# Performance work log

Hardware: AMD Instinct MI355X
Metric: run time of the kernel (lower is better)

Reference implementation:

```python
import jax, jax.numpy as jnp
import numpy as np

N_NODES = 100000
N_EDGES = 1600000
IN_CH, OUT_CH = 6, 32


def _glorot(key, shape):
    fan_in, fan_out = shape[0], shape[1]
    lim = float(np.sqrt(6.0 / (fan_in + fan_out)))
    return jax.random.uniform(key, shape, jnp.float32, -lim, lim)


def setup_inputs() -> dict:
    key = jax.random.key(0)
    ks = jax.random.split(key, 16)
    x = jax.random.normal(ks[0], (N_NODES, IN_CH), jnp.float32)
    edge_tp = jax.random.randint(ks[1], (2, N_EDGES), 0, N_NODES, jnp.int32)
    edge_int = jax.random.randint(ks[2], (2, N_EDGES), 0, N_NODES, jnp.int32)
    return {
        'x': x, 'edge_tp': edge_tp, 'edge_int': edge_int,
        # block 1 (6 -> 32): self lin, per-edge-type message lins, residual proj
        'W_self1': _glorot(ks[3], (IN_CH, OUT_CH)), 'b1': jnp.zeros((OUT_CH,), jnp.float32),
        'W_tp1': _glorot(ks[4], (IN_CH, OUT_CH)), 'W_int1': _glorot(ks[5], (IN_CH, OUT_CH)),
        'W_res1': _glorot(ks[6], (IN_CH, OUT_CH)),
        # block 2 (32 -> 32): identity residual
        'W_self2': _glorot(ks[7], (OUT_CH, OUT_CH)), 'b2': jnp.zeros((OUT_CH,), jnp.float32),
        'W_tp2': _glorot(ks[8], (OUT_CH, OUT_CH)), 'W_int2': _glorot(ks[9], (OUT_CH, OUT_CH)),
        # instance decoder MLP
        'Wd1': _glorot(ks[10], (OUT_CH, OUT_CH)), 'bd1': jnp.zeros((OUT_CH,), jnp.float32),
        'Wd2': _glorot(ks[11], (OUT_CH, 1)), 'bd2': jnp.zeros((1,), jnp.float32),
    }


def _hetero_block(x, edge_tp, edge_int, W_self, b, W_tp, W_int, W_res):
    """One ResidualGeneralHeteroConvBlock: per-edge-type message passing
    ('temp_previous' -> sum-agg, 'intersects' -> mean-agg) + self transform +
    residual, then ReLU. x: [N, Cin]."""
    N = x.shape[0]
    # temp_previous: add reducer
    src, dst = edge_tp[0], edge_tp[1]
    m_tp = jax.ops.segment_sum(x[src] @ W_tp, dst, num_segments=N)  # [N, Cout]
    # intersects: mean reducer
    s2, d2 = edge_int[0], edge_int[1]
    m_sum = jax.ops.segment_sum(x[s2] @ W_int, d2, num_segments=N)
    cnt = jax.ops.segment_sum(jnp.ones(d2.shape, x.dtype), d2, num_segments=N)
    m_int = m_sum / jnp.maximum(cnt, 1.0)[:, None]
    res = x @ W_res if W_res is not None else x
    return jax.nn.relu(x @ W_self + b + m_tp + m_int + res)


def reference(x, edge_tp, edge_int,
              W_self1, b1, W_tp1, W_int1, W_res1,
              W_self2, b2, W_tp2, W_int2,
              Wd1, bd1, Wd2, bd2):
    h = _hetero_block(x, edge_tp, edge_int, W_self1, b1, W_tp1, W_int1, W_res1)
    h = _hetero_block(h, edge_tp, edge_int, W_self2, b2, W_tp2, W_int2, None)
    # instance decoder: Linear -> ReLU -> Linear -> sigmoid
    h = jax.nn.relu(h @ Wd1 + bd1)
    return jax.nn.sigmoid(h @ Wd2 + bd2)  # [N, 1]
```

## Files before the change

kernel.cpp:

```cpp
#include <hip/hip_runtime.h>
#include <hip/hip_bf16.h>
#include <math.h>

#define NN   100000
#define ICH  6
#define OCH  32
#define NBK  782
#define PBLK 512
#define CAPB 4720
#define CAPL 4800
#define GN   16
#define CHMAX 6272

#define WPREP_N 4480

typedef float f32x2 __attribute__((ext_vector_type(2)));
typedef float f32x4 __attribute__((ext_vector_type(4)));

__device__ __forceinline__ void pk_fma(f32x2& a, f32x2 x, f32x2 y) {
    asm("v_pk_fma_f32 %0, %1, %2, %0" : "+v"(a) : "v"(x), "v"(y));
}
__device__ __forceinline__ f32x2 pk_add(f32x2 x, f32x2 y) {
    f32x2 d;
    asm("v_pk_add_f32 %0, %1, %2" : "=v"(d) : "v"(x), "v"(y));
    return d;
}

__device__ __forceinline__ float ldf(const void* p, long i, int f32) {
    return f32 ? ((const float*)p)[i]
               : __bfloat162float(((const __hip_bfloat16*)p)[i]);
}
__device__ __forceinline__ float lo16f(unsigned u) { return __uint_as_float(u << 16); }
__device__ __forceinline__ float hi16f(unsigned u) { return __uint_as_float(u & 0xFFFF0000u); }

__device__ __forceinline__ int binof(int n, int s) {
    return ((n >> 7) << 8) | (s << 7) | (n & 127);
}

__global__ __launch_bounds__(1024) void partAx_r25(
        const int* __restrict__ src_tp, const int* __restrict__ dst_tp,
        const int* __restrict__ src_int, const int* __restrict__ dst_int,
        int Etp, int E,
        const void* __restrict__ x, unsigned* __restrict__ xw,
        int* __restrict__ gcnt, unsigned* __restrict__ part,
        int* __restrict__ flagp,
        const void* Ws2, const void* b2v, const void* Wt2, const void* Wi2,
        const void* Wd1, const void* bd1v, const void* Wd2, const void* bd2v,
        float* __restrict__ wprep) {
    __shared__ unsigned rawv[CHMAX];
    __shared__ unsigned short rawb[CHMAX];
    __shared__ unsigned sorted[CHMAX];
    __shared__ int lh[NBK];
    __shared__ int cur[NBK];
    __shared__ int lofs[NBK + 1];
    __shared__ int wsum[16];
    __shared__ int weird;
    int t = threadIdx.x, blk = blockIdx.x;
    if (t == 0) weird = 0;
    for (int b = t; b < NBK; b += 1024) lh[b] = 0;
    __syncthreads();
    {
        const __hip_bfloat16* p = (const __hip_bfloat16*)x;
        int w = 0;
        for (int i = t; i < 4096; i += 1024) {
            float v = fabsf(__bfloat162float(p[i]));
            if (!(v <= 1000.0f) || (v > 0.0f && v < 1e-4f)) w++;
        }
        if (w) atomicAdd(&weird, w);
    }
    __syncthreads();
    int f32 = (weird > 500) ? 1 : 0;
    if (blk == 0 && t == 0) *flagp = f32;
    if (blk == 0) {
        for (int i = t; i < 96 * 32; i += 1024) {
            int k = i >> 5, c = i & 31;
            float w;
            if (k < 32)      w = ldf(Ws2, k * 32 + c, f32) + ((k == c) ? 1.0f : 0.0f);
            else if (k < 64) w = ldf(Wt2, (k - 32) * 32 + c, f32);
            else             w = ldf(Wi2, (k - 64) * 32 + c, f32);
            wprep[c * 100 + k] = w;
        }
        for (int i = t; i < 32 * 32; i += 1024) {
            int k = i >> 5, c = i & 31;
            wprep[3200 + c * 36 + k] = ldf(Wd1, k * 32 + c, f32);
        }
        if (t < 32) {
            wprep[4352 + t]      = ldf(b2v, t, f32);
            wprep[4352 + 32 + t] = ldf(bd1v, t, f32);
            wprep[4352 + 64 + t] = ldf(Wd2, t, f32);
        }
        if (t == 0) wprep[4352 + 96] = ldf(bd2v, 0, f32);
    }
    for (int w = blk * 1024 + t; w < NN * 4; w += PBLK * 1024) {
        int n = w >> 2, j = w & 3;
        int c0 = 2 * j, c1 = 2 * j + 1;
        __hip_bfloat16 v0 = (c0 < ICH) ? __float2bfloat16(ldf(x, (long)n * ICH + c0, f32))
                                       : __float2bfloat16(0.0f);
        __hip_bfloat16 v1 = (c1 < ICH) ? __float2bfloat16(ldf(x, (long)n * ICH + c1, f32))
                                       : __float2bfloat16(0.0f);
        xw[w] = (unsigned)__bfloat16_as_ushort(v0) |
                ((unsigned)__bfloat16_as_ushort(v1) << 16);
    }
    int CH = (E + PBLK - 1) / PBLK;
    int lo = blk * CH, hi = min(E, lo + CH);
    int n = hi - lo;
    for (int e = lo + t; e < hi; e += 1024) {
        int bin, src;
        if (e < Etp) { bin = binof(dst_tp[e], 0); src = src_tp[e]; }
        else         { bin = binof(dst_int[e - Etp], 1); src = src_int[e - Etp]; }
        int i = e - lo;
        rawv[i] = ((unsigned)(bin & 255) << 24) | (unsigned)src;
        rawb[i] = (unsigned short)(bin >> 8);
        atomicAdd(&lh[bin >> 8], 1);
    }
    __syncthreads();
    for (int b = t; b < NBK; b += 1024) {
        int cnt = lh[b];
        cur[b] = b * CAPB + (cnt ? atomicAdd(&gcnt[b], cnt) : 0);
    }
    {
        int v = (t < NBK) ? lh[t] : 0;
        int lane = t & 63, w = t >> 6;
        int s = v;
#pragma unroll
        for (int d = 1; d < 64; d <<= 1) {
            int u = __shfl_up(s, d, 64);
            if (lane >= d) s += u;
        }
        if (lane == 63) wsum[w] = s;
        __syncthreads();
        int prefix = 0;
#pragma unroll
        for (int j = 0; j < 16; ++j) prefix += (j < w) ? wsum[j] : 0;
        int excl = prefix + s - v;
        if (t < NBK) {
            lofs[t] = excl;
            cur[t] -= excl;
            lh[t]  = excl;
        }
        if (t == 0) lofs[NBK] = n;
        __syncthreads();
    }
    for (int i = t; i < n; i += 1024) {
        int b = rawb[i];
        int pos = atomicAdd(&lh[b], 1);
        sorted[pos] = rawv[i];
    }
    __syncthreads();
    {
        int grp = t >> 3, lane8 = t & 7;
        for (int b = grp; b < NBK; b += 128) {
            int st = lofs[b], en = lofs[b + 1];
            int dst = cur[b];
            for (int i = st + lane8; i < en; i += 8)
                part[dst + i] = sorted[i];
        }
    }
}

__global__ __launch_bounds__(256) void passBn1_r25(
        unsigned* __restrict__ partcsr, const int* __restrict__ gcnt,
        int* __restrict__ off, int* __restrict__ end,
        const unsigned* __restrict__ xw,
        const void* Ws1, const void* b1v, const void* Wt1, const void* Wi1, const void* Wr1,
        unsigned* __restrict__ h1u, float* __restrict__ invc_a,
        const int* __restrict__ flag) {
    __shared__ unsigned lp[CAPL];
    __shared__ unsigned sorted[CAPL];
    __shared__ int scnt[256], obin[256];
    __shared__ int wsum4[4];
    __shared__ float agg[256][7];
    __shared__ float sWs[ICH][32], sWt[ICH][32], sWi[ICH][32];
    __shared__ float sb1[32];
    int k = blockIdx.x, t = threadIdx.x;
    int f32 = *flag;
    if (k == 0 && t < 16) h1u[(size_t)NN * 16u + t] = 0u;
    if (t < ICH * OCH) {
        int kk = t >> 5, c = t & 31;
        sWs[kk][c] = ldf(Ws1, t, f32) + ldf(Wr1, t, f32);
        sWt[kk][c] = ldf(Wt1, t, f32);
        sWi[kk][c] = ldf(Wi1, t, f32);
    }
    if (t < 32) sb1[t] = ldf(b1v, t, f32);
    int s0 = k * CAPB;
    int cnt = gcnt[k]; if (cnt > CAPB) cnt = CAPB;
    scnt[t] = 0;
    __syncthreads();
    for (int i = t; i < cnt; i += 256) {
        unsigned v = partcsr[s0 + i];
        lp[i] = v;
        atomicAdd(&scnt[v >> 24], 1);
    }
    __syncthreads();
    int own = scnt[t];
    obin[t] = own;
    int excl;
    {
        int lane = t & 63, w = t >> 6;
        int s = own;
#pragma unroll
        for (int d = 1; d < 64; d <<= 1) {
            int u = __shfl_up(s, d, 64);
            if (lane >= d) s += u;
        }
        if (lane == 63) wsum4[w] = s;
        __syncthreads();
        int prefix = 0;
#pragma unroll
        for (int j = 0; j < 4; ++j) prefix += (j < w) ? wsum4[j] : 0;
        excl = prefix + s - own;
    }
    scnt[t] = excl;
    off[k * 256 + t] = s0 + excl;
    end[k * 256 + t] = s0 + excl + own;
    __syncthreads();
    for (int i = t; i < cnt; i += 256) {
        unsigned v = lp[i];
        int pos = atomicAdd(&scnt[v >> 24], 1);
        sorted[pos] = v & 0xFFFFFFu;
    }
    __syncthreads();
    for (int i = t; i < cnt; i += 256) partcsr[s0 + i] = sorted[i];
    float a0 = 0, a1 = 0, a2 = 0, a3 = 0, a4 = 0, a5 = 0;
    {
        int i = excl, e = excl + own;
        for (; i + 4 <= e; i += 4) {
            unsigned q0 = sorted[i], q1 = sorted[i + 1];
            unsigned q2 = sorted[i + 2], q3 = sorted[i + 3];
            uint4 u0 = *(const uint4*)(xw + q0 * 4u);
            uint4 u1 = *(const uint4*)(xw + q1 * 4u);
            uint4 u2 = *(const uint4*)(xw + q2 * 4u);
            uint4 u3 = *(const uint4*)(xw + q3 * 4u);
            a0 += lo16f(u0.x) + lo16f(u1.x) + lo16f(u2.x) + lo16f(u3.x);
            a1 += hi16f(u0.x) + hi16f(u1.x) + hi16f(u2.x) + hi16f(u3.x);
            a2 += lo16f(u0.y) + lo16f(u1.y) + lo16f(u2.y) + lo16f(u3.y);
            a3 += hi16f(u0.y) + hi16f(u1.y) + hi16f(u2.y) + hi16f(u3.y);
            a4 += lo16f(u0.z) + lo16f(u1.z) + lo16f(u2.z) + lo16f(u3.z);
            a5 += hi16f(u0.z) + hi16f(u1.z) + hi16f(u2.z) + hi16f(u3.z);
        }
        for (; i < e; ++i) {
            uint4 u = *(const uint4*)(xw + sorted[i] * 4u);
            a0 += lo16f(u.x); a1 += hi16f(u.x);
            a2 += lo16f(u.y); a3 += hi16f(u.y);
            a4 += lo16f(u.z); a5 += hi16f(u.z);
        }
    }
    agg[t][0] = a0; agg[t][1] = a1; agg[t][2] = a2;
    agg[t][3] = a3; agg[t][4] = a4; agg[t][5] = a5;
    __syncthreads();

    int nl = t & 127, half = t >> 7;
    int node = k * 128 + nl;
    if (node < NN) {
        int degi = obin[128 + nl];
        float invc = 1.0f / fmaxf((float)degi, 1.0f);
        if (half == 0) invc_a[node] = invc;
        uint4 us = *(const uint4*)(xw + (unsigned)node * 4u);
        float xv[ICH] = {lo16f(us.x), hi16f(us.x), lo16f(us.y),
                         hi16f(us.y), lo16f(us.z), hi16f(us.z)};
        float aT[ICH], aI[ICH];
#pragma unroll
        for (int q = 0; q < ICH; ++q) {
            aT[q] = agg[nl][q];
            aI[q] = agg[128 + nl][q] * invc;
        }
        unsigned row[8];
#pragma unroll
        for (int cc = 0; cc < 8; ++cc) {
            int c0 = half * 16 + 2 * cc, c1 = c0 + 1;
            float v0 = sb1[c0], v1 = sb1[c1];
#pragma unroll
            for (int q = 0; q < ICH; ++q) {
                v0 += xv[q] * sWs[q][c0] + aT[q] * sWt[q][c0] + aI[q] * sWi[q][c0];
                v1 += xv[q] * sWs[q][c1] + aT[q] * sWt[q][c1] + aI[q] * sWi[q][c1];
            }
            unsigned w0 = (unsigned)__bfloat16_as_ushort(__float2bfloat16(fmaxf(v0, 0.0f)));
            unsigned w1 = (unsigned)__bfloat16_as_ushort(__float2bfloat16(fmaxf(v1, 0.0f)));
            row[cc] = w0 | (w1 << 16);
        }
        unsigned base = (unsigned)node * 16u + (unsigned)half * 8u;
        *(uint4*)(h1u + base)      = make_uint4(row[0], row[1], row[2], row[3]);
        *(uint4*)(h1u + base + 4u) = make_uint4(row[4], row[5], row[6], row[7]);
    }
}

__global__ __launch_bounds__(512, 8) void final_r25(
        const unsigned* __restrict__ h1u,
        const int* __restrict__ csr, const int* __restrict__ off,
        const int* __restrict__ end,
        const float* __restrict__ invc,
        const float* __restrict__ wprep,
        void* __restrict__ out, const int* __restrict__ flag) {
    __shared__ float wsh[WPREP_N];
    __shared__ float sv[GN][100];
    int t = threadIdx.x;
    int f32 = *flag;
    {
        const float4* wp4 = (const float4*)wprep;
        float4* ws4 = (float4*)wsh;
        for (int i = t; i < WPREP_N / 4; i += 512) ws4[i] = wp4[i];
    }
    __syncthreads();

    int g = t >> 5, c = t & 31;
    int sub = c >> 3, r = c & 7;
    int half = c >> 4, l = c & 15;
    int node = blockIdx.x * GN + g;

    unsigned uself = h1u[(unsigned)node * 16u + l];
    float ic = invc[node];
    int binA = ((node >> 7) << 8) | (node & 127);
    int binB = binA | 128;
    int sa0 = off[binA], sa1 = end[binA];
    int sb0 = off[binB], sb1_ = end[binB];
    int ma0 = sa1 - sa0; if (ma0 > 32) ma0 = 32;
    int mb0 = sb1_ - sb0; if (mb0 > 32) mb0 = 32;
    int idxA = (ma0 > 0) ? csr[sa0 + (c < ma0 ? c : ma0 - 1)] : 0;
    int idxB = (mb0 > 0) ? csr[sb0 + (c < mb0 ? c : mb0 - 1)] : 0;

    if (half == 0)
        *(float2*)&sv[g][2 * l] = make_float2(lo16f(uself), hi16f(uself));

    f32x2 va0 = {0.f, 0.f}, va1 = va0;
    f32x2 vb0 = va0, vb1 = va0;
    int sA = sa0, sB = sb0;
    while (sA < sa1 || sB < sb1_) {
        int mA = sa1 - sA; if (mA > 32) mA = 32;
        int mB = sb1_ - sB; if (mB > 32) mB = 32;
        int nA = sA + 32, nB = sB + 32;
        int nmA = sa1 - nA; if (nmA > 32) nmA = 32;
        int nmB = sb1_ - nB; if (nmB > 32) nmB = 32;
        int nidxA = (nmA > 0) ? csr[nA + (c < nmA ? c : nmA - 1)] : 0;
        int nidxB = (nmB > 0) ? csr[nB + (c < nmB ? c : nmB - 1)] : 0;
        int mx = mA > mB ? mA : mB;
        for (int b = 0; b < mx; b += 16) {
            uint2 uA[4], uB[4];
#pragma unroll
            for (int q = 0; q < 4; ++q) {
                int e = b + 4 * q + sub;
                int sj = __shfl(idxA, e & 31, 32);
                sj = (e < mA) ? sj : NN;
                uA[q] = *(const uint2*)(h1u + (unsigned)sj * 16u + 2u * r);
            }
#pragma unroll
            for (int q = 0; q < 4; ++q) {
                int e = b + 4 * q + sub;
                int sj = __shfl(idxB, e & 31, 32);
                sj = (e < mB) ? sj : NN;
                uB[q] = *(const uint2*)(h1u + (unsigned)sj * 16u + 2u * r);
            }
#pragma unroll
            for (int q = 0; q < 4; ++q) {
                f32x2 x0 = {lo16f(uA[q].x), hi16f(uA[q].x)};
                f32x2 x1 = {lo16f(uA[q].y), hi16f(uA[q].y)};
                va0 = pk_add(va0, x0); va1 = pk_add(va1, x1);
            }
#pragma unroll
            for (int q = 0; q < 4; ++q) {
                f32x2 x0 = {lo16f(uB[q].x), hi16f(uB[q].x)};
                f32x2 x1 = {lo16f(uB[q].y), hi16f(uB[q].y)};
                vb0 = pk_add(vb0, x0); vb1 = pk_add(vb1, x1);
            }
        }
        idxA = nidxA; idxB = nidxB; sA = nA; sB = nB;
    }
#pragma unroll
    for (int sh = 8; sh <= 16; sh <<= 1) {
        va0.x += __shfl_down(va0.x, sh, 32); va0.y += __shfl_down(va0.y, sh, 32);
        va1.x += __shfl_down(va1.x, sh, 32); va1.y += __shfl_down(va1.y, sh, 32);
        vb0.x += __shfl_down(vb0.x, sh, 32); vb0.y += __shfl_down(vb0.y, sh, 32);
        vb1.x += __shfl_down(vb1.x, sh, 32); vb1.y += __shfl_down(vb1.y, sh, 32);
    }
    if (c < 8) {
        *(float2*)&sv[g][32 + 4 * r]     = make_float2(va0.x, va0.y);
        *(float2*)&sv[g][32 + 4 * r + 2] = make_float2(va1.x, va1.y);
        *(float2*)&sv[g][64 + 4 * r]     = make_float2(vb0.x * ic, vb0.y * ic);
        *(float2*)&sv[g][64 + 4 * r + 2] = make_float2(vb1.x * ic, vb1.y * ic);
    }

    const float* svg  = sv[g];
    const float* wrow = wsh + c * 100;
    f32x2 acc = {wsh[4352 + c], 0.f};
#pragma unroll 4
    for (int k = 0; k < 96; k += 4) {
        f32x4 s4 = *(const f32x4*)(svg + k);
        f32x4 w4 = *(const f32x4*)(wrow + k);
        pk_fma(acc, __builtin_shufflevector(s4, s4, 0, 1),
                    __builtin_shufflevector(w4, w4, 0, 1));
        pk_fma(acc, __builtin_shufflevector(s4, s4, 2, 3),
                    __builtin_shufflevector(w4, w4, 2, 3));
    }
    float h2 = fmaxf(acc.x + acc.y, 0.0f);
    sv[g][c] = h2;

    const float* wdrow = wsh + 3200 + c * 36;
    f32x2 acc2 = {wsh[4352 + 32 + c], 0.f};
#pragma unroll 4
    for (int k = 0; k < 32; k += 4) {
        f32x4 s4 = *(const f32x4*)(svg + k);
        f32x4 w4 = *(const f32x4*)(wdrow + k);
        pk_fma(acc2, __builtin_shufflevector(s4, s4, 0, 1),
                     __builtin_shufflevector(w4, w4, 0, 1));
        pk_fma(acc2, __builtin_shufflevector(s4, s4, 2, 3),
                     __builtin_shufflevector(w4, w4, 2, 3));
    }
    float h3 = fmaxf(acc2.x + acc2.y, 0.0f);

    float p = h3 * wsh[4352 + 64 + c];
#pragma unroll
    for (int offs = 16; offs; offs >>= 1) p += __shfl_down(p, offs, 32);
    if (c == 0) {
        float z = p + wsh[4352 + 96];
        float sgm = 1.0f / (1.0f + expf(-z));
        if (f32) ((float*)out)[node] = sgm;
        else     ((__hip_bfloat16*)out)[node] = __float2bfloat16(sgm);
    }
}

extern "C" void kernel_launch(void* const* d_in, const int* in_sizes, int n_in,
                              void* d_out, int out_size, void* d_ws, size_t ws_size,
                              hipStream_t stream) {
    const void* x      = d_in[0];
    const int* edge_tp = (const int*)d_in[1];
    const int* edge_int= (const int*)d_in[2];
    const void* Ws1 = d_in[3], *b1 = d_in[4], *Wt1 = d_in[5], *Wi1 = d_in[6], *Wr1 = d_in[7];
    const void* Ws2 = d_in[8], *b2 = d_in[9];
    const void* Wt2 = d_in[10], *Wi2 = d_in[11];
    const void* Wd1 = d_in[12], *bd1 = d_in[13], *Wd2 = d_in[14], *bd2 = d_in[15];

    const int E_tp  = in_sizes[1] / 2;
    const int E_int = in_sizes[2] / 2;

    int*      flag    = (int*)d_ws;
    int*      gcnt    = flag + 64;
    int*      off     = gcnt + 1024;
    int*      end     = off + 200448;
    unsigned* xw      = (unsigned*)(end + 200448);
    unsigned* partcsr = xw + (size_t)4 * NN;
    unsigned* h1u     = partcsr + (size_t)NBK * CAPB;
    float*    invc    = (float*)(h1u + (size_t)16 * (NN + 1));
    float*    wprep   = invc + NN;

    const int* src_tp  = edge_tp;
    const int* dst_tp  = edge_tp + E_tp;
    const int* src_int = edge_int;
    const int* dst_int = edge_int + E_int;

    hipMemsetAsync(gcnt, 0, NBK * sizeof(int), stream);

    partAx_r25<<<PBLK, 1024, 0, stream>>>(src_tp, dst_tp, src_int, dst_int,
                                          E_tp, E_tp + E_int, x, xw, gcnt,
                                          partcsr, flag,
                                          Ws2, b2, Wt2, Wi2, Wd1, bd1, Wd2, bd2,
                                          wprep);
    passBn1_r25<<<NBK, 256, 0, stream>>>(partcsr, gcnt, off, end, xw,
                                         Ws1, b1, Wt1, Wi1, Wr1,
                                         h1u, invc, flag);

    final_r25<<<NN / GN, 512, 0, stream>>>(h1u, (const int*)partcsr, off, end, invc,
                                           wprep, d_out, flag);
}
```

Before: 214.3 us.

## Split layer-2 gather into two channel-half passes with persistent blocks

Stores h1 as two separate 16-channel halves and runs the layer-2 neighbor gather in two phases per node group, each touching only one half-array. The aim is a smaller working set (about 3.2MB per half) that fits better in cache for the random gathers. The final kernel becomes a persistent grid of 768 blocks, each looping over up to 9 node groups and keeping partial matmul sums in shared memory. The cost is walking the CSR twice, reading the index lists again, and lower parallelism per block.

New measurement: 263.4 us. 22.9% more time.

```diff
diff --git a/kernel.cpp b/kernel.cpp
--- a/kernel.cpp
+++ b/kernel.cpp
@@ -11,6 +11,9 @@
 #define CAPL 4800
 #define GN   16
 #define CHMAX 6272
+#define NGRP 6250
+#define FGRID 768
+#define GPB 9
 
 #define WPREP_N 4480
 
@@ -37,7 +40,7 @@
     return ((n >> 7) << 8) | (s << 7) | (n & 127);
 }
 
-__global__ __launch_bounds__(1024) void partAx_r25(
+__global__ __launch_bounds__(1024) void partAx_r27(
         const int* __restrict__ src_tp, const int* __restrict__ dst_tp,
         const int* __restrict__ src_int, const int* __restrict__ dst_int,
         int Etp, int E,
@@ -72,24 +75,28 @@
     int f32 = (weird > 500) ? 1 : 0;
     if (blk == 0 && t == 0) *flagp = f32;
     if (blk == 0) {
-        for (int i = t; i < 96 * 32; i += 1024) {
-            int k = i >> 5, c = i & 31;
+        for (int i = t; i < 3072; i += 1024) {
+            int half = (i >= 1536) ? 1 : 0;
+            int r = i - half * 1536;
+            int c = r / 48, j = r % 48;
+            int k = (j < 16) ? j : (j < 32 ? 32 + (j - 16) : 64 + (j - 32));
+            k += half * 16;
             float w;
             if (k < 32)      w = ldf(Ws2, k * 32 + c, f32) + ((k == c) ? 1.0f : 0.0f);
             else if (k < 64) w = ldf(Wt2, (k - 32) * 32 + c, f32);
             else             w = ldf(Wi2, (k - 64) * 32 + c, f32);
-            wprep[c * 100 + k] = w;
+            wprep[half * 1536 + c * 48 + j] = w;
         }
         for (int i = t; i < 32 * 32; i += 1024) {
             int k = i >> 5, c = i & 31;
-            wprep[3200 + c * 36 + k] = ldf(Wd1, k * 32 + c, f32);
+            wprep[3072 + c * 36 + k] = ldf(Wd1, k * 32 + c, f32);
         }
         if (t < 32) {
-            wprep[4352 + t]      = ldf(b2v, t, f32);
-            wprep[4352 + 32 + t] = ldf(bd1v, t, f32);
-            wprep[4352 + 64 + t] = ldf(Wd2, t, f32);
-        }
-        if (t == 0) wprep[4352 + 96] = ldf(bd2v, 0, f32);
+            wprep[4224 + t] = ldf(b2v, t, f32);
+            wprep[4256 + t] = ldf(bd1v, t, f32);
+            wprep[4288 + t] = ldf(Wd2, t, f32);
+        }
+        if (t == 0) wprep[4320] = ldf(bd2v, 0, f32);
     }
     for (int w = blk * 1024 + t; w < NN * 4; w += PBLK * 1024) {
         int n = w >> 2, j = w & 3;
@@ -158,13 +165,13 @@
     }
 }
 
-__global__ __launch_bounds__(256) void passBn1_r25(
+__global__ __launch_bounds__(256) void passBn1_r27(
         unsigned* __restrict__ partcsr, const int* __restrict__ gcnt,
         int* __restrict__ off, int* __restrict__ end,
         const unsigned* __restrict__ xw,
         const void* Ws1, const void* b1v, const void* Wt1, const void* Wi1, const void* Wr1,
-        unsigned* __restrict__ h1u, float* __restrict__ invc_a,
-        const int* __restrict__ flag) {
+        unsigned* __restrict__ h1lo, unsigned* __restrict__ h1hi,
+        float* __restrict__ invc_a, const int* __restrict__ flag) {
     __shared__ unsigned lp[CAPL];
     __shared__ unsigned sorted[CAPL];
     __shared__ int scnt[256], obin[256];
@@ -174,7 +181,10 @@
     __shared__ float sb1[32];
     int k = blockIdx.x, t = threadIdx.x;
     int f32 = *flag;
-    if (k == 0 && t < 16) h1u[(size_t)NN * 16u + t] = 0u;
+    if (k == 0) {
+        if (t < 8)              h1lo[(size_t)NN * 8u + t] = 0u;
+        else if (t < 16)        h1hi[(size_t)NN * 8u + (t - 8)] = 0u;
+    }
     if (t < ICH * OCH) {
         int kk = t >> 5, c = t & 31;
         sWs[kk][c] = ldf(Ws1, t, f32) + ldf(Wr1, t, f32);
@@ -278,37 +288,22 @@
             unsigned w1 = (unsigned)__bfloat16_as_ushort(__float2bfloat16(fmaxf(v1, 0.0f)));
             row[cc] = w0 | (w1 << 16);
         }
-        unsigned base = (unsigned)node * 16u + (unsigned)half * 8u;
-        *(uint4*)(h1u + base)      = make_uint4(row[0], row[1], row[2], row[3]);
-        *(uint4*)(h1u + base + 4u) = make_uint4(row[4], row[5], row[6], row[7]);
-    }
-}
-
-__global__ __launch_bounds__(512, 8) void final_r25(
-        const unsigned* __restrict__ h1u,
-        const int* __restrict__ csr, const int* __restrict__ off,
-        const int* __restrict__ end,
-        const float* __restrict__ invc,
-        const float* __restrict__ wprep,
-        void* __restrict__ out, const int* __restrict__ flag) {
-    __shared__ float wsh[WPREP_N];
-    __shared__ float sv[GN][100];
-    int t = threadIdx.x;
-    int f32 = *flag;
-    {
-        const float4* wp4 = (const float4*)wprep;
-        float4* ws4 = (float4*)wsh;
-        for (int i = t; i < WPREP_N / 4; i += 512) ws4[i] = wp4[i];
-    }
-    __syncthreads();
-
-    int g = t >> 5, c = t & 31;
-    int sub = c >> 3, r = c & 7;
-    int half = c >> 4, l = c & 15;
-    int node = blockIdx.x * GN + g;
-
-    unsigned uself = h1u[(unsigned)node * 16u + l];
-    float ic = invc[node];
+        unsigned* hb = (half ? h1hi : h1lo) + (unsigned)node * 8u;
+        *(uint4*)(hb)      = make_uint4(row[0], row[1], row[2], row[3]);
+        *(uint4*)(hb + 4u) = make_uint4(row[4], row[5], row[6], row[7]);
+    }
+}
+
+__device__ __forceinline__ float half_phase(
+        const unsigned* __restrict__ hp, const int* __restrict__ csr,
+        const int* __restrict__ off, const int* __restrict__ end,
+        float ic, int node, float* __restrict__ svg,
+        const float* __restrict__ wrow, float accin, int c) {
+    int sub8 = c >> 2, r4 = c & 3;
+    if (c < 8) {
+        unsigned uu = hp[(unsigned)node * 8u + c];
+        svg[2 * c] = lo16f(uu); svg[2 * c + 1] = hi16f(uu);
+    }
     int binA = ((node >> 7) << 8) | (node & 127);
     int binB = binA | 128;
     int sa0 = off[binA], sa1 = end[binA];
@@ -318,11 +313,7 @@
     int idxA = (ma0 > 0) ? csr[sa0 + (c < ma0 ? c : ma0 - 1)] : 0;
     int idxB = (mb0 > 0) ? csr[sb0 + (c < mb0 ? c : mb0 - 1)] : 0;
 
-    if (half == 0)
-        *(float2*)&sv[g][2 * l] = make_float2(lo16f(uself), hi16f(uself));
-
-    f32x2 va0 = {0.f, 0.f}, va1 = va0;
-    f32x2 vb0 = va0, vb1 = va0;
+    f32x2 va0 = {0.f, 0.f}, va1 = va0, vb0 = va0, vb1 = va0;
     int sA = sa0, sB = sb0;
     while (sA < sa1 || sB < sb1_) {
         int mA = sa1 - sA; if (mA > 32) mA = 32;
@@ -332,57 +323,51 @@
         int nmB = sb1_ - nB; if (nmB > 32) nmB = 32;
         int nidxA = (nmA > 0) ? csr[nA + (c < nmA ? c : nmA - 1)] : 0;
         int nidxB = (nmB > 0) ? csr[nB + (c < nmB ? c : nmB - 1)] : 0;
-        int mx = mA > mB ? mA : mB;
-        for (int b = 0; b < mx; b += 16) {
-            uint2 uA[4], uB[4];
-#pragma unroll
-            for (int q = 0; q < 4; ++q) {
-                int e = b + 4 * q + sub;
-                int sj = __shfl(idxA, e & 31, 32);
-                sj = (e < mA) ? sj : NN;
-                uA[q] = *(const uint2*)(h1u + (unsigned)sj * 16u + 2u * r);
-            }
-#pragma unroll
-            for (int q = 0; q < 4; ++q) {
-                int e = b + 4 * q + sub;
-                int sj = __shfl(idxB, e & 31, 32);
-                sj = (e < mB) ? sj : NN;
-                uB[q] = *(const uint2*)(h1u + (unsigned)sj * 16u + 2u * r);
-            }
-#pragma unroll
-            for (int q = 0; q < 4; ++q) {
-                f32x2 x0 = {lo16f(uA[q].x), hi16f(uA[q].x)};
-                f32x2 x1 = {lo16f(uA[q].y), hi16f(uA[q].y)};
-                va0 = pk_add(va0, x0); va1 = pk_add(va1, x1);
-            }
-#pragma unroll
-            for (int q = 0; q < 4; ++q) {
-                f32x2 x0 = {lo16f(uB[q].x), hi16f(uB[q].x)};
-                f32x2 x1 = {lo16f(uB[q].y), hi16f(uB[q].y)};
-                vb0 = pk_add(vb0, x0); vb1 = pk_add(vb1, x1);
-            }
+        uint2 uA[4], uB[4];
+#pragma unroll
+        for (int q = 0; q < 4; ++q) {
+            int e = 8 * q + sub8;
+            int sj = __shfl(idxA, e, 32);
+            sj = (e < mA) ? sj : NN;
+            uA[q] = *(const uint2*)(hp + (unsigned)sj * 8u + 2u * r4);
+        }
+#pragma unroll
+        for (int q = 0; q < 4; ++q) {
+            int e = 8 * q + sub8;
+            int sj = __shfl(idxB, e, 32);
+            sj = (e < mB) ? sj : NN;
+            uB[q] = *(const uint2*)(hp + (unsigned)sj * 8u + 2u * r4);
+        }
+#pragma unroll
+        for (int q = 0; q < 4; ++q) {
+            f32x2 x0 = {lo16f(uA[q].x), hi16f(uA[q].x)};
+            f32x2 x1 = {lo16f(uA[q].y), hi16f(uA[q].y)};
+            va0 = pk_add(va0, x0); va1 = pk_add(va1, x1);
+        }
+#pragma unroll
+        for (int q = 0; q < 4; ++q) {
+            f32x2 x0 = {lo16f(uB[q].x), hi16f(uB[q].x)};
+            f32x2 x1 = {lo16f(uB[q].y), hi16f(uB[q].y)};
+            vb0 = pk_add(vb0, x0); vb1 = pk_add(vb1, x1);
         }
         idxA = nidxA; idxB = nidxB; sA = nA; sB = nB;
     }
 #pragma unroll
-    for (int sh = 8; sh <= 16; sh <<= 1) {
+    for (int sh = 4; sh <= 16; sh <<= 1) {
         va0.x += __shfl_down(va0.x, sh, 32); va0.y += __shfl_down(va0.y, sh, 32);
         va1.x += __shfl_down(va1.x, sh, 32); va1.y += __shfl_down(va1.y, sh, 32);
         vb0.x += __shfl_down(vb0.x, sh, 32); vb0.y += __shfl_down(vb0.y, sh, 32);
         vb1.x += __shfl_down(vb1.x, sh, 32); vb1.y += __shfl_down(vb1.y, sh, 32);
     }
-    if (c < 8) {
-        *(float2*)&sv[g][32 + 4 * r]     = make_float2(va0.x, va0.y);
-        *(float2*)&sv[g][32 + 4 * r + 2] = make_float2(va1.x, va1.y);
-        *(float2*)&sv[g][64 + 4 * r]     = make_float2(vb0.x * ic, vb0.y * ic);
-        *(float2*)&sv[g][64 + 4 * r + 2] = make_float2(vb1.x * ic, vb1.y * ic);
-    }
-
-    const float* svg  = sv[g];
-    const float* wrow = wsh + c * 100;
-    f32x2 acc = {wsh[4352 + c], 0.f};
-#pragma unroll 4
-    for (int k = 0; k < 96; k += 4) {
+    if (c < 4) {
+        *(float2*)&svg[16 + 4 * c]     = make_float2(va0.x, va0.y);
+        *(float2*)&svg[16 + 4 * c + 2] = make_float2(va1.x, va1.y);
+        *(float2*)&svg[32 + 4 * c]     = make_float2(vb0.x * ic, vb0.y * ic);
+        *(float2*)&svg[32 + 4 * c + 2] = make_float2(vb1.x * ic, vb1.y * ic);
+    }
+    f32x2 acc = {accin, 0.f};
+#pragma unroll
+    for (int k = 0; k < 48; k += 4) {
         f32x4 s4 = *(const f32x4*)(svg + k);
         f32x4 w4 = *(const f32x4*)(wrow + k);
         pk_fma(acc, __builtin_shufflevector(s4, s4, 0, 1),
@@ -390,30 +375,67 @@
         pk_fma(acc, __builtin_shufflevector(s4, s4, 2, 3),
                     __builtin_shufflevector(w4, w4, 2, 3));
     }
-    float h2 = fmaxf(acc.x + acc.y, 0.0f);
-    sv[g][c] = h2;
-
-    const float* wdrow = wsh + 3200 + c * 36;
-    f32x2 acc2 = {wsh[4352 + 32 + c], 0.f};
-#pragma unroll 4
-    for (int k = 0; k < 32; k += 4) {
-        f32x4 s4 = *(const f32x4*)(svg + k);
-        f32x4 w4 = *(const f32x4*)(wdrow + k);
-        pk_fma(acc2, __builtin_shufflevector(s4, s4, 0, 1),
-                     __builtin_shufflevector(w4, w4, 0, 1));
-        pk_fma(acc2, __builtin_shufflevector(s4, s4, 2, 3),
-                     __builtin_shufflevector(w4, w4, 2, 3));
-    }
-    float h3 = fmaxf(acc2.x + acc2.y, 0.0f);
-
-    float p = h3 * wsh[4352 + 64 + c];
-#pragma unroll
-    for (int offs = 16; offs; offs >>= 1) p += __shfl_down(p, offs, 32);
-    if (c == 0) {
-        float z = p + wsh[4352 + 96];
-        float sgm = 1.0f / (1.0f + expf(-z));
-        if (f32) ((float*)out)[node] = sgm;
-        else     ((__hip_bfloat16*)out)[node] = __float2bfloat16(sgm);
+    return acc.x + acc.y;
+}
+
+__global__ __launch_bounds__(512, 8) void final2p_r27(
+        const unsigned* __restrict__ h1lo, const unsigned* __restrict__ h1hi,
+        const int* __restrict__ csr, const int* __restrict__ off,
+        const int* __restrict__ end, const float* __restrict__ invc,
+        const float* __restrict__ wprep, void* __restrict__ out,
+        const int* __restrict__ flag) {
+    __shared__ float wsh[WPREP_N];
+    __shared__ float sv[GN][48];
+    __shared__ float part[GPB][GN][32];
+    int t = threadIdx.x, blk = blockIdx.x;
+    int f32 = *flag;
+    {
+        const float4* wp4 = (const float4*)wprep;
+        float4* ws4 = (float4*)wsh;
+        for (int i = t; i < WPREP_N / 4; i += 512) ws4[i] = wp4[i];
+    }
+    __syncthreads();
+    int g = t >> 5, c = t & 31;
+
+    for (int gi = 0; gi < GPB; ++gi) {
+        int grp = gi * FGRID + blk;
+        if (grp >= NGRP) continue;
+        int node = grp * GN + g;
+        float ic = invc[node];
+        part[gi][g][c] = half_phase(h1lo, csr, off, end, ic, node, sv[g],
+                                    wsh + c * 48, wsh[4224 + c], c);
+    }
+    for (int gi = 0; gi < GPB; ++gi) {
+        int grp = gi * FGRID + blk;
+        if (grp >= NGRP) continue;
+        int node = grp * GN + g;
+        float ic = invc[node];
+        float acc = half_phase(h1hi, csr, off, end, ic, node, sv[g],
+                               wsh + 1536 + c * 48, part[gi][g][c], c);
+        float h2 = fmaxf(acc, 0.0f);
+        sv[g][c] = h2;
+        const float* svg = sv[g];
+        const float* wdrow = wsh + 3072 + c * 36;
+        f32x2 acc2 = {wsh[4256 + c], 0.f};
+#pragma unroll
+        for (int k = 0; k < 32; k += 4) {
+            f32x4 s4 = *(const f32x4*)(svg + k);
+            f32x4 w4 = *(const f32x4*)(wdrow + k);
+            pk_fma(acc2, __builtin_shufflevector(s4, s4, 0, 1),
+                         __builtin_shufflevector(w4, w4, 0, 1));
+            pk_fma(acc2, __builtin_shufflevector(s4, s4, 2, 3),
+                         __builtin_shufflevector(w4, w4, 2, 3));
+        }
+        float h3 = fmaxf(acc2.x + acc2.y, 0.0f);
+        float p = h3 * wsh[4288 + c];
+#pragma unroll
+        for (int offs = 16; offs; offs >>= 1) p += __shfl_down(p, offs, 32);
+        if (c == 0) {
+            float z = p + wsh[4320];
+            float sgm = 1.0f / (1.0f + expf(-z));
+            if (f32) ((float*)out)[node] = sgm;
+            else     ((__hip_bfloat16*)out)[node] = __float2bfloat16(sgm);
+        }
     }
 }
 
@@ -437,8 +459,9 @@
     int*      end     = off + 200448;
     unsigned* xw      = (unsigned*)(end + 200448);
     unsigned* partcsr = xw + (size_t)4 * NN;
-    unsigned* h1u     = partcsr + (size_t)NBK * CAPB;
-    float*    invc    = (float*)(h1u + (size_t)16 * (NN + 1));
+    unsigned* h1lo    = partcsr + (size_t)NBK * CAPB;
+    unsigned* h1hi    = h1lo + (size_t)8 * (NN + 1);
+    float*    invc    = (float*)(h1hi + (size_t)8 * (NN + 1));
     float*    wprep   = invc + NN;
 
     const int* src_tp  = edge_tp;
@@ -448,15 +471,15 @@
 
     hipMemsetAsync(gcnt, 0, NBK * sizeof(int), stream);
 
-    partAx_r25<<<PBLK, 1024, 0, stream>>>(src_tp, dst_tp, src_int, dst_int,
+    partAx_r27<<<PBLK, 1024, 0, stream>>>(src_tp, dst_tp, src_int, dst_int,
                                           E_tp, E_tp + E_int, x, xw, gcnt,
                                           partcsr, flag,
                                           Ws2, b2, Wt2, Wi2, Wd1, bd1, Wd2, bd2,
                                           wprep);
-    passBn1_r25<<<NBK, 256, 0, stream>>>(partcsr, gcnt, off, end, xw,
+    passBn1_r27<<<NBK, 256, 0, stream>>>(partcsr, gcnt, off, end, xw,
                                          Ws1, b1, Wt1, Wi1, Wr1,
-                                         h1u, invc, flag);
-
-    final_r25<<<NN / GN, 512, 0, stream>>>(h1u, (const int*)partcsr, off, end, invc,
-                                           wprep, d_out, flag);
-}
+                                         h1lo, h1hi, invc, flag);
+
+    final2p_r27<<<FGRID, 512, 0, stream>>>(h1lo, h1hi, (const int*)partcsr,
+                                           off, end, invc, wprep, d_out, flag);
+}
```
